# Kernel optimization log

Measured on AMD Instinct MI355X. Metric: run time of the kernel, lower is better.

## Reference

```python
import jax, jax.numpy as jnp
import numpy as np

GAMMA = 0.95  # usage decay from NTM.__init__

def setup_inputs() -> dict:
    key = jax.random.key(0)
    ks = jax.random.split(key, 16)
    B, N, M, R, U, Din = 256, 32768, 64, 4, 256, 512
    Dc = Din + R * M  # controller input = x concat prev read vectors
    s = 0.02
    x = jax.random.normal(ks[0], (B, Din), jnp.float32)
    A = jax.random.normal(ks[1], (N, M), jnp.float32) * 0.1
    wr_prev = jax.nn.softmax(jax.random.normal(ks[2], (R, B, N), jnp.float32), axis=-1)
    wu_prev = jax.random.uniform(ks[3], (B, N), jnp.float32)
    read_prev = jax.random.normal(ks[4], (R, B, M), jnp.float32) * 0.1
    h = jax.random.normal(ks[5], (B, U), jnp.float32) * 0.1
    c = jax.random.normal(ks[6], (B, U), jnp.float32) * 0.1
    W = jax.random.normal(ks[7], (Dc, 4 * U), jnp.float32) * s
    Uw = jax.random.normal(ks[8], (U, 4 * U), jnp.float32) * s
    b = jnp.zeros((4 * U,), jnp.float32)
    Wk = jax.random.normal(ks[9], (R, U, M), jnp.float32) * s
    bk = jnp.zeros((R, M), jnp.float32)
    Wa = jax.random.normal(ks[10], (U, R), jnp.float32) * s
    ba = jnp.zeros((R,), jnp.float32)
    return dict(x=x, A=A, wr_prev=wr_prev, wu_prev=wu_prev, read_prev=read_prev,
                h=h, c=c, W=W, Uw=Uw, b=b, Wk=Wk, bk=bk, Wa=Wa, ba=ba)

def reference(x, A, wr_prev, wu_prev, read_prev, h, c, W, Uw, b, Wk, bk, Wa, ba):
    B, N = wu_prev.shape
    R, _, M = read_prev.shape
    # ---- controller (single LSTM cell step, keras gate order i,f,g,o) ----
    ctrl_in = jnp.concatenate([x, read_prev.transpose(1, 0, 2).reshape(B, -1)], axis=-1)
    gates = ctrl_in @ W + h @ Uw + b
    gi, gf, gg, go = jnp.split(gates, 4, axis=-1)
    c_new = jax.nn.sigmoid(gf) * c + jax.nn.sigmoid(gi) * jnp.tanh(gg)
    h_new = jax.nn.sigmoid(go) * jnp.tanh(c_new)  # controller_output [B,U]
    # ---- least-used weights from previous usage ----
    least = jnp.argmin(wu_prev, axis=-1)                       # [B]
    wlu = jax.nn.one_hot(least, N, dtype=wu_prev.dtype)        # [B,N]
    # ---- read heads: cosine-similarity content addressing ----
    kt = jnp.tanh(jnp.einsum('bu,rum->rbm', h_new, Wk) + bk[:, None, :])  # [R,B,M]
    inner = jnp.einsum('rbm,nm->rbn', kt, A)                   # [R,B,N]
    knorm = jnp.linalg.norm(kt, axis=-1)                       # [R,B]
    anorm = jnp.linalg.norm(A, axis=-1)                        # [N]
    Ksim = inner / (knorm[..., None] * anorm[None, None, :] + 1e-16)
    wr = jax.nn.softmax(Ksim, axis=-1)                         # [R,B,N]
    # ---- write head: gated mix of prev read weights and least-used ----
    alpha = jax.nn.sigmoid(jnp.tanh(h_new @ Wa + ba))          # [B,R]
    a = alpha.T[:, :, None]                                    # [R,B,1]
    ww = a * wr_prev + (1.0 - a) * wlu[None]                   # [R,B,N]
    # ---- usage update ----
    wu = GAMMA * wu_prev + jnp.sum(wr + ww, axis=0)            # [B,N]
    # ---- memory: erase least-used row(s), then tanh additive writes ----
    erase = 1.0 - jnp.max(wlu, axis=0)                         # [N]
    A_new = A * erase[:, None]
    for r in range(R):  # small fixed head count
        A_new = jnp.tanh(A_new + jnp.einsum('bn,bm->nm', ww[r], kt[r]))
    # ---- reads and output ----
    reads = jnp.einsum('rbn,nm->rbm', wr, A_new)               # [R,B,M]
    out = jnp.concatenate([h_new, reads.transpose(1, 0, 2).reshape(B, -1)], axis=-1)
    return out
```

## Files before the change

### kernel.cpp

```cpp
#include <hip/hip_runtime.h>
#include <hip/hip_bf16.h>
#include <stdint.h>

#define B_   256
#define N_   32768
#define M_   64
#define R_   4
#define U_   256
#define DIN_ 512
#define DC_  768
#define J4_  1024
#define Q_   1024
#define NPART_ 64

typedef __attribute__((ext_vector_type(8))) short short8v;
typedef __attribute__((ext_vector_type(4))) float f32x4;

__device__ __forceinline__ float sigm(float x){ return 1.f/(1.f+__expf(-x)); }
__device__ __forceinline__ float tanh_f(float x){ float e=__expf(2.f*x); return 1.f - 2.f/(e+1.f); }
__device__ __forceinline__ unsigned short f2bf(float x){
    unsigned u = __float_as_uint(x);
    u += 0x7FFFu + ((u>>16)&1u);
    return (unsigned short)(u>>16);
}

__global__ __launch_bounds__(256) void k_zero(int* lflag, float* l){
    int i = blockIdx.x*256 + threadIdx.x;
    if(i < N_) lflag[i] = 0;
    if(i < Q_) l[i] = 0.f;
}

__global__ __launch_bounds__(256) void k_anorm(const float* A, float* anorm, unsigned short* A_bf){
    int n = blockIdx.x*4 + (threadIdx.x>>6);
    int lane = threadIdx.x & 63;
    float v = A[n*64 + lane];
    A_bf[n*64 + lane] = f2bf(v);
    float s = v*v;
    #pragma unroll
    for(int m=1;m<64;m<<=1) s += __shfl_xor(s, m, 64);
    if(lane==0) anorm[n] = sqrtf(s);
}

__global__ __launch_bounds__(256) void k_argmin(const float* wu, int* least, int* lflag){
    __shared__ float sv[256]; __shared__ int si[256];
    int b = blockIdx.x, t = threadIdx.x;
    const float* row = wu + (size_t)b*N_;
    float bv = 3.4e38f; int bi = 0;
    for(int n=t; n<N_; n+=256){ float v = row[n]; if(v < bv){ bv=v; bi=n; } }
    sv[t]=bv; si[t]=bi; __syncthreads();
    for(int s=128;s>0;s>>=1){
        if(t<s){
            float ov=sv[t+s]; int oi=si[t+s];
            if(ov<sv[t] || (ov==sv[t] && oi<si[t])){ sv[t]=ov; si[t]=oi; }
        }
        __syncthreads();
    }
    if(t==0){ least[b]=si[0]; lflag[si[0]]=1; }
}

__global__ __launch_bounds__(256) void k_lstm_gemm(const float* x, const float* rp, const float* h,
                                                   const float* W, const float* Uw, float* gpart){
    __shared__ float s_in[8*64];
    int bt = blockIdx.x >> 4, ks = blockIdx.x & 15;
    int b0 = bt*8, t = threadIdx.x;
    #pragma unroll
    for(int i=t; i<512; i+=256){
        int bb = i>>6, kk = i&63, b = b0+bb;
        float v;
        if(ks < 8)       v = x[b*DIN_ + ks*64 + kk];
        else if(ks < 12) v = rp[(size_t)(ks-8)*(B_*M_) + b*64 + kk];
        else             v = h[b*U_ + (ks-12)*64 + kk];
        s_in[bb*64 + kk] = v;
    }
    __syncthreads();
    float4 acc[8];
    #pragma unroll
    for(int i=0;i<8;i++) acc[i] = make_float4(0.f,0.f,0.f,0.f);
    const float* Wsel; int krel;
    if(ks < 12){ Wsel = W; krel = ks*64; } else { Wsel = Uw; krel = (ks-12)*64; }
    int j0 = t*4;
    #pragma unroll 4
    for(int kk=0; kk<64; kk++){
        float4 w = *(const float4*)(Wsel + (size_t)(krel+kk)*J4_ + j0);
        #pragma unroll
        for(int bb=0;bb<8;bb++){
            float s = s_in[bb*64 + kk];
            acc[bb].x += s*w.x; acc[bb].y += s*w.y; acc[bb].z += s*w.z; acc[bb].w += s*w.w;
        }
    }
    #pragma unroll
    for(int bb=0;bb<8;bb++)
        *(float4*)(gpart + (size_t)ks*(B_*J4_) + (size_t)(b0+bb)*J4_ + j0) = acc[bb];
}

__global__ __launch_bounds__(256) void k_lstm_act(const float* gpart, const float* bias, const float* c,
                                                  float* h_new, float* out){
    int b = blockIdx.x, u = threadIdx.x;
    float gi=bias[u], gf=bias[256+u], gg=bias[512+u], go=bias[768+u];
    #pragma unroll
    for(int s=0;s<16;s++){
        const float* gp = gpart + (size_t)s*(B_*J4_) + (size_t)b*J4_;
        gi += gp[u]; gf += gp[256+u]; gg += gp[512+u]; go += gp[768+u];
    }
    float cn = sigm(gf)*c[b*U_+u] + sigm(gi)*tanh_f(gg);
    float hn = sigm(go)*tanh_f(cn);
    h_new[b*U_+u] = hn;
    out[(size_t)b*512 + u] = hn;
}

__global__ __launch_bounds__(64) void k_kta(const float* h_new, const float* Wk, const float* bk,
                                            const float* Wa, const float* ba,
                                            float* kt, unsigned short* kt_bf, unsigned short* aktT,
                                            float* alpha, float* knorm){
    __shared__ float h_l[256];
    int r = blockIdx.x >> 8, b = blockIdx.x & 255, m = threadIdx.x;
    for(int i=m;i<256;i+=64) h_l[i] = h_new[b*U_ + i];
    __syncthreads();
    float acc = bk[r*64 + m];
    const float* wkp = Wk + (size_t)r*U_*M_ + m;
    for(int u=0;u<256;u++) acc += h_l[u] * wkp[u*64];
    float k = tanh_f(acc);
    float s = k*k;
    #pragma unroll
    for(int mm=1;mm<64;mm<<=1) s += __shfl_xor(s, mm, 64);
    float pa = 0.f;
    #pragma unroll
    for(int uu=0; uu<4; uu++){ int u = m*4+uu; pa += h_l[u]*Wa[u*R_ + r]; }
    #pragma unroll
    for(int mm=1;mm<64;mm<<=1) pa += __shfl_xor(pa, mm, 64);
    float al = sigm(tanh_f(pa + ba[r]));
    int q = r*256 + b;
    kt[q*64 + m]    = k;
    kt_bf[q*64 + m] = f2bf(k);
    aktT[(size_t)(r*64 + m)*256 + b] = f2bf(al*k);
    if(m==0){ knorm[q] = sqrtf(s); alpha[q] = al; }
}

__global__ __launch_bounds__(256) void k_Gfused(const float* wrp, const unsigned short* aktT,
                                                const float* A, const float* kt, const float* alpha,
                                                const int* least, const int* lflag,
                                                unsigned short* Vt){
    __shared__ __align__(16) char wrl[16384];
    __shared__ __align__(16) char aktl[16384];
    __shared__ int least_l[256];
    int nb = blockIdx.x*64, t = threadIdx.x;
    int w = t>>6, lane = t&63;
    int r16 = lane&15, hq = lane>>4;
    for(int i=t;i<256;i+=256) least_l[i] = least[i];

    f32x4 acc[4][4];
    #pragma unroll
    for(int r=0;r<4;r++)
        #pragma unroll
        for(int ms=0;ms<4;ms++) acc[r][ms] = (f32x4){0.f,0.f,0.f,0.f};

    int sb = lane>>1, nh = (lane&1)*32;
    for(int kt8=0; kt8<8; kt8++){
        int b0 = kt8*32;
        __syncthreads();
        const float4* src = (const float4*)(wrp + ((size_t)w*B_ + b0 + sb)*N_ + nb + nh);
        float4 f[8];
        #pragma unroll
        for(int i=0;i<8;i++) f[i] = src[i];
        const uint4* ap = (const uint4*)(aktT + ((size_t)(w*64 + lane))*256 + b0);
        uint4 av[4];
        #pragma unroll
        for(int c=0;c<4;c++) av[c] = ap[c];
        #pragma unroll
        for(int i=0;i<8;i++){
            float vv[4] = {f[i].x, f[i].y, f[i].z, f[i].w};
            #pragma unroll
            for(int c=0;c<4;c++){
                int n = nh + i*4 + c;
                *(unsigned short*)(wrl + n*256 + ((w*64 + sb*2) ^ ((n&7)<<4))) = f2bf(vv[c]);
            }
        }
        #pragma unroll
        for(int c=0;c<4;c++)
            *(uint4*)(aktl + lane*256 + ((w*64 + c*16) ^ ((lane&7)<<4))) = av[c];
        __syncthreads();
        #pragma unroll
        for(int r=0;r<4;r++){
            int n = w*16 + r16;
            short8v af = *(const short8v*)(wrl + n*256 + ((r*64 + hq*16) ^ ((n&7)<<4)));
            #pragma unroll
            for(int ms=0;ms<4;ms++){
                int m = ms*16 + r16;
                short8v bf = *(const short8v*)(aktl + m*256 + ((r*64 + hq*16) ^ ((m&7)<<4)));
                acc[r][ms] = __builtin_amdgcn_mfma_f32_16x16x32_bf16(af, bf, acc[r][ms], 0, 0, 0);
            }
        }
    }
    __syncthreads();
    #pragma unroll
    for(int j=0;j<4;j++){
        int nl = w*16 + hq*4 + j, gn = nb + nl;
        int fl = lflag[gn];
        float er = fl ? 0.f : 1.f;
        float sadd[4][4];
        #pragma unroll
        for(int r=0;r<4;r++){ sadd[r][0]=0.f; sadd[r][1]=0.f; sadd[r][2]=0.f; sadd[r][3]=0.f; }
        if(fl){
            for(int b=0;b<256;b++){
                if(least_l[b]==gn){
                    #pragma unroll
                    for(int r=0;r<4;r++){
                        float am = 1.f - alpha[r*256+b];
                        const float* kp = kt + ((size_t)(r*256+b))*64 + r16;
                        #pragma unroll
                        for(int ms=0;ms<4;ms++) sadd[r][ms] += am * kp[ms*16];
                    }
                }
            }
        }
        #pragma unroll
        for(int ms=0;ms<4;ms++){
            int m = ms*16 + r16;
            float v = A[(size_t)gn*64 + m] * er;
            #pragma unroll
            for(int r=0;r<4;r++) v = tanh_f(v + acc[r][ms][j] + sadd[r][ms]);
            *(unsigned short*)(wrl + m*128 + ((nl*2) ^ ((m&7)<<4))) = f2bf(v);
        }
    }
    __syncthreads();
    int m = t>>2, cq = t&3;
    #pragma unroll
    for(int hh=0;hh<2;hh++){
        uint4 v = *(const uint4*)(wrl + m*128 + ((cq*32 + hh*16) ^ ((m&7)<<4)));
        *(uint4*)(Vt + (size_t)m*N_ + nb + cq*16 + hh*8) = v;
    }
}

__global__ __launch_bounds__(256) void k_attn(const unsigned short* kt_bf, const unsigned short* A_bf,
                                              const unsigned short* Vt, const float* knorm,
                                              const float* anorm, float* part, float* l){
    __shared__ __align__(16) unsigned short Pl[64*256];
    int nc = blockIdx.x >> 4, qt = blockIdx.x & 15;
    int qb = qt*64, nb = nc*512;
    int lane = threadIdx.x & 63, w = threadIdx.x >> 6;
    int r16 = lane & 15, hq = lane >> 4;
    const short8v* kp = (const short8v*)(kt_bf + (size_t)(qb + w*16 + r16)*64 + hq*8);
    short8v ka0 = kp[0], ka1 = kp[4];
    float kn[4];
    #pragma unroll
    for(int j=0;j<4;j++) kn[j] = knorm[qb + w*16 + hq*4 + j];
    f32x4 O[4];
    #pragma unroll
    for(int mt=0;mt<4;mt++) O[mt] = (f32x4){0.f,0.f,0.f,0.f};
    float lp[4] = {0.f,0.f,0.f,0.f};
    int g2 = (r16 >> 2) & 3;

    for(int c=0; c<2; c++){
        int n0c = nb + c*256;
        __syncthreads();
        for(int nt=0; nt<16; nt++){
            int ntb = n0c + nt*16;
            const short8v* bp = (const short8v*)(A_bf + (size_t)(ntb + r16)*64 + hq*8);
            f32x4 acc = (f32x4){0.f,0.f,0.f,0.f};
            acc = __builtin_amdgcn_mfma_f32_16x16x32_bf16(ka0, bp[0], acc, 0, 0, 0);
            acc = __builtin_amdgcn_mfma_f32_16x16x32_bf16(ka1, bp[4], acc, 0, 0, 0);
            float an = anorm[ntb + r16];
            unsigned um[4];
            #pragma unroll
            for(int j=0;j<4;j++){
                float p = __expf(__fdividef(acc[j], kn[j]*an + 1e-16f));
                lp[j] += p;
                um[j] = (unsigned)f2bf(p);
            }
            int nl = nt*16 + (r16 & ~1);
            #pragma unroll
            for(int j=0;j<4;j++){
                unsigned up = __shfl_xor((int)um[j], 1, 64);
                if((lane & 1) == 0){
                    unsigned word = um[j] | (up << 16);
                    int byteoff = (w*16 + hq*4 + j)*512 + ((nl ^ (hq<<4)) << 1);
                    *(unsigned*)((char*)Pl + byteoff) = word;
                }
            }
        }
        __syncthreads();
        #pragma unroll 2
        for(int ks=0; ks<8; ks++){
            short8v pa = *(const short8v*)((const char*)Pl +
                          ((w*16 + r16)*512 + (((ks*32 + hq*8) ^ (g2<<4)) << 1)));
            #pragma unroll
            for(int mt=0; mt<4; mt++){
                const short8v* vp = (const short8v*)(Vt + (size_t)(mt*16 + r16)*N_ + n0c + ks*32 + hq*8);
                O[mt] = __builtin_amdgcn_mfma_f32_16x16x32_bf16(pa, vp[0], O[mt], 0, 0, 0);
            }
        }
    }
    #pragma unroll
    for(int mt=0; mt<4; mt++)
        #pragma unroll
        for(int j=0;j<4;j++)
            part[((size_t)nc*Q_ + (qb + w*16 + hq*4 + j))*64 + mt*16 + r16] = O[mt][j];
    #pragma unroll
    for(int j=0;j<4;j++){
        #pragma unroll
        for(int m2=1;m2<16;m2<<=1) lp[j] += __shfl_xor(lp[j], m2, 64);
        if(r16 == 0) atomicAdd(l + qb + w*16 + hq*4 + j, lp[j]);
    }
}

__global__ __launch_bounds__(256) void k_reduce(const float* part, const float* l, float* out){
    int tg = blockIdx.x*256 + threadIdx.x;
    int q = tg >> 6, m = tg & 63;
    float s = 0.f;
    for(int cc=0;cc<NPART_;cc++) s += part[(size_t)cc*(Q_*64) + tg];
    float val = s / l[q];
    int r = q >> 8, b = q & 255;
    out[(size_t)b*512 + 256 + r*64 + m] = val;
}

extern "C" void kernel_launch(void* const* d_in, const int* in_sizes, int n_in,
                              void* d_out, int out_size, void* d_ws, size_t ws_size,
                              hipStream_t stream) {
    const float* x        = (const float*)d_in[0];
    const float* A        = (const float*)d_in[1];
    const float* wr_prev  = (const float*)d_in[2];
    const float* wu_prev  = (const float*)d_in[3];
    const float* read_prev= (const float*)d_in[4];
    const float* h        = (const float*)d_in[5];
    const float* c        = (const float*)d_in[6];
    const float* W        = (const float*)d_in[7];
    const float* Uw       = (const float*)d_in[8];
    const float* bvec     = (const float*)d_in[9];
    const float* Wk       = (const float*)d_in[10];
    const float* bk       = (const float*)d_in[11];
    const float* Wa       = (const float*)d_in[12];
    const float* ba       = (const float*)d_in[13];
    float* out = (float*)d_out;

    char* wsp = (char*)d_ws;
    float* gpart  = (float*)(wsp);
    float* part   = (float*)(wsp + 16777216);
    unsigned short* A_bf  = (unsigned short*)(wsp + 33554432);
    unsigned short* Vt_bf = (unsigned short*)(wsp + 37748736);
    unsigned short* aktT  = (unsigned short*)(wsp + 41943040);
    float* kt     = (float*)(wsp + 42074112);
    unsigned short* kt_bf = (unsigned short*)(wsp + 42336256);
    float* h_new  = (float*)(wsp + 42467328);
    float* alpha  = (float*)(wsp + 42729472);
    float* knorm  = (float*)(wsp + 42733568);
    float* anorm  = (float*)(wsp + 42737664);
    int*   lflag  = (int*)  (wsp + 42868736);
    float* l      = (float*)(wsp + 42999808);
    int*   least  = (int*)  (wsp + 43003904);

    k_zero     <<<128, 256, 0, stream>>>(lflag, l);
    k_anorm    <<<8192,256, 0, stream>>>(A, anorm, A_bf);
    k_argmin   <<<256, 256, 0, stream>>>(wu_prev, least, lflag);
    k_lstm_gemm<<<512, 256, 0, stream>>>(x, read_prev, h, W, Uw, gpart);
    k_lstm_act <<<256, 256, 0, stream>>>(gpart, bvec, c, h_new, out);
    k_kta      <<<1024, 64, 0, stream>>>(h_new, Wk, bk, Wa, ba, kt, kt_bf, aktT, alpha, knorm);
    k_Gfused   <<<512, 256, 0, stream>>>(wr_prev, aktT, A, kt, alpha, least, lflag, Vt_bf);
    k_attn     <<<1024,256, 0, stream>>>(kt_bf, A_bf, Vt_bf, knorm, anorm, part, l);
    k_reduce   <<<256, 256, 0, stream>>>(part, l, out);
}
```

Before: 453.3 us.

## Load MFMA operands directly from global in k_Gfused, dropping LDS staging

Reworks the write-contribution matmul kernel so each lane gathers its wr_prev column values and aktT fragments straight from global memory into MFMA operand registers. This removes the per-iteration LDS staging buffers and both __syncthreads barriers, and cuts shared memory use to a small output stage, which may raise occupancy. The cost is strided, poorly coalesced global loads: eight rows N apart per lane for wr_prev, plus repeated aktT loads across waves. Unroll pragmas are also added to two small reduction loops.

```diff
diff --git a/kernel.cpp b/kernel.cpp
--- a/kernel.cpp
+++ b/kernel.cpp
@@ -22,6 +22,9 @@
     unsigned u = __float_as_uint(x);
     u += 0x7FFFu + ((u>>16)&1u);
     return (unsigned short)(u>>16);
+}
+__device__ __forceinline__ unsigned pack_bf2(float lo, float hi){
+    return (unsigned)f2bf(lo) | ((unsigned)f2bf(hi) << 16);
 }
 
 __global__ __launch_bounds__(256) void k_zero(int* lflag, float* l){
@@ -118,6 +121,7 @@
     __syncthreads();
     float acc = bk[r*64 + m];
     const float* wkp = Wk + (size_t)r*U_*M_ + m;
+    #pragma unroll 8
     for(int u=0;u<256;u++) acc += h_l[u] * wkp[u*64];
     float k = tanh_f(acc);
     float s = k*k;
@@ -140,8 +144,7 @@
                                                 const float* A, const float* kt, const float* alpha,
                                                 const int* least, const int* lflag,
                                                 unsigned short* Vt){
-    __shared__ __align__(16) char wrl[16384];
-    __shared__ __align__(16) char aktl[16384];
+    __shared__ __align__(16) char vstage[8192];
     __shared__ int least_l[256];
     int nb = blockIdx.x*64, t = threadIdx.x;
     int w = t>>6, lane = t&63;
@@ -154,40 +157,24 @@
         #pragma unroll
         for(int ms=0;ms<4;ms++) acc[r][ms] = (f32x4){0.f,0.f,0.f,0.f};
 
-    int sb = lane>>1, nh = (lane&1)*32;
+    int n_g = nb + w*16 + r16;
+    #pragma unroll 2
     for(int kt8=0; kt8<8; kt8++){
         int b0 = kt8*32;
-        __syncthreads();
-        const float4* src = (const float4*)(wrp + ((size_t)w*B_ + b0 + sb)*N_ + nb + nh);
-        float4 f[8];
-        #pragma unroll
-        for(int i=0;i<8;i++) f[i] = src[i];
-        const uint4* ap = (const uint4*)(aktT + ((size_t)(w*64 + lane))*256 + b0);
-        uint4 av[4];
-        #pragma unroll
-        for(int c=0;c<4;c++) av[c] = ap[c];
-        #pragma unroll
-        for(int i=0;i<8;i++){
-            float vv[4] = {f[i].x, f[i].y, f[i].z, f[i].w};
-            #pragma unroll
-            for(int c=0;c<4;c++){
-                int n = nh + i*4 + c;
-                *(unsigned short*)(wrl + n*256 + ((w*64 + sb*2) ^ ((n&7)<<4))) = f2bf(vv[c]);
-            }
-        }
-        #pragma unroll
-        for(int c=0;c<4;c++)
-            *(uint4*)(aktl + lane*256 + ((w*64 + c*16) ^ ((lane&7)<<4))) = av[c];
-        __syncthreads();
         #pragma unroll
         for(int r=0;r<4;r++){
-            int n = w*16 + r16;
-            short8v af = *(const short8v*)(wrl + n*256 + ((r*64 + hq*16) ^ ((n&7)<<4)));
+            const float* colp = wrp + ((size_t)(r*B_ + b0 + hq*8))*N_ + n_g;
+            float v0 = colp[0];        float v1 = colp[(size_t)N_];
+            float v2 = colp[2*(size_t)N_]; float v3 = colp[3*(size_t)N_];
+            float v4 = colp[4*(size_t)N_]; float v5 = colp[5*(size_t)N_];
+            float v6 = colp[6*(size_t)N_]; float v7 = colp[7*(size_t)N_];
+            union { short8v s; unsigned u[4]; } af;
+            af.u[0] = pack_bf2(v0,v1); af.u[1] = pack_bf2(v2,v3);
+            af.u[2] = pack_bf2(v4,v5); af.u[3] = pack_bf2(v6,v7);
             #pragma unroll
             for(int ms=0;ms<4;ms++){
-                int m = ms*16 + r16;
-                short8v bf = *(const short8v*)(aktl + m*256 + ((r*64 + hq*16) ^ ((m&7)<<4)));
-                acc[r][ms] = __builtin_amdgcn_mfma_f32_16x16x32_bf16(af, bf, acc[r][ms], 0, 0, 0);
+                short8v bf = *(const short8v*)(aktT + ((size_t)(r*64 + ms*16 + r16))*256 + b0 + hq*8);
+                acc[r][ms] = __builtin_amdgcn_mfma_f32_16x16x32_bf16(af.s, bf, acc[r][ms], 0, 0, 0);
             }
         }
     }
@@ -219,14 +206,14 @@
             float v = A[(size_t)gn*64 + m] * er;
             #pragma unroll
             for(int r=0;r<4;r++) v = tanh_f(v + acc[r][ms][j] + sadd[r][ms]);
-            *(unsigned short*)(wrl + m*128 + ((nl*2) ^ ((m&7)<<4))) = f2bf(v);
+            *(unsigned short*)(vstage + m*128 + ((nl*2) ^ ((m&7)<<4))) = f2bf(v);
         }
     }
     __syncthreads();
     int m = t>>2, cq = t&3;
     #pragma unroll
     for(int hh=0;hh<2;hh++){
-        uint4 v = *(const uint4*)(wrl + m*128 + ((cq*32 + hh*16) ^ ((m&7)<<4)));
+        uint4 v = *(const uint4*)(vstage + m*128 + ((cq*32 + hh*16) ^ ((m&7)<<4)));
         *(uint4*)(Vt + (size_t)m*N_ + nb + cq*16 + hh*8) = v;
     }
 }
@@ -307,6 +294,7 @@
     int tg = blockIdx.x*256 + threadIdx.x;
     int q = tg >> 6, m = tg & 63;
     float s = 0.f;
+    #pragma unroll 8
     for(int cc=0;cc<NPART_;cc++) s += part[(size_t)cc*(Q_*64) + tg];
     float val = s / l[q];
     int r = q >> 8, b = q & 255;
```

After: 465.8 us. 2.8% more time.
